# Kernel optimization log

Hardware: AMD Instinct MI355X
Metric: run time of the kernel (lower is better)

## Reference

```python
import jax, jax.numpy as jnp
import numpy as np

B, HW, ENC, DEC, ATTN = 512, 196, 2048, 512, 512

def setup_inputs() -> dict:
    key = jax.random.key(0)
    ks = jax.random.split(key, 8)
    s_enc = 1.0 / np.sqrt(ENC)
    s_dec = 1.0 / np.sqrt(DEC)
    s_v = 1.0 / np.sqrt(ATTN)
    return {
        "enc_out": jax.random.normal(ks[0], (B, HW, ENC), dtype=jnp.float32),
        "dec_h": jax.random.normal(ks[1], (B, DEC), dtype=jnp.float32),
        "W_enc": jax.random.uniform(ks[2], (ENC, ATTN), jnp.float32, -s_enc, s_enc),
        "b_enc": jax.random.uniform(ks[3], (ATTN,), jnp.float32, -s_enc, s_enc),
        "W_dec": jax.random.uniform(ks[4], (DEC, ATTN), jnp.float32, -s_dec, s_dec),
        "b_dec": jax.random.uniform(ks[5], (ATTN,), jnp.float32, -s_dec, s_dec),
        "W_v": jax.random.uniform(ks[6], (ATTN,), jnp.float32, -s_v, s_v),
        "b_v": jax.random.uniform(ks[7], (), jnp.float32, -s_v, s_v),
    }

def reference(enc_out, dec_h, W_enc, b_enc, W_dec, b_dec, W_v, b_v):
    # attn1: [B, HW, ATTN]; attn2: [B, 1, ATTN]
    attn1 = jnp.einsum('bse,ea->bsa', enc_out, W_enc) + b_enc
    attn2 = (dec_h @ W_dec + b_dec)[:, None, :]
    score = jax.nn.relu(attn1 + attn2)
    logits = jnp.einsum('bsa,a->bs', score, W_v) + b_v  # [B, HW]
    alpha = jax.nn.softmax(logits, axis=1)
    context_vec = jnp.einsum('bs,bse->be', alpha, enc_out)
    return (context_vec, alpha)
```

## Files before the change

kernel.cpp:

```cpp
#include <hip/hip_runtime.h>
#include <hip/hip_bf16.h>
#include <cstdint>
#include <cstddef>

#define B_    512
#define HW_   196
#define ENC_  2048
#define DEC_  512
#define ATTN_ 512
#define M_    (B_*HW_)

typedef __attribute__((ext_vector_type(8))) short short8;
typedef __attribute__((ext_vector_type(4))) float f32x4;

__device__ __forceinline__ unsigned short f2bf(float x) {
  __bf16 b = (__bf16)x;
  return __builtin_bit_cast(unsigned short, b);
}
__device__ __forceinline__ unsigned int cvt2(float x, float y) {
  return (unsigned)f2bf(x) | ((unsigned)f2bf(y) << 16);
}

__device__ __forceinline__ void gload_lds16(const void* g, void* l) {
  __builtin_amdgcn_global_load_lds(
      (const __attribute__((address_space(1))) void*)g,
      (__attribute__((address_space(3))) void*)l, 16, 0, 0);
}

__global__ __launch_bounds__(256)
void k_convert(const float* __restrict__ in, unsigned short* __restrict__ out) {
  const size_t total  = (size_t)M_ * ENC_;
  const size_t stride = (size_t)gridDim.x * 256 * 8;
  for (size_t i = ((size_t)blockIdx.x * 256 + threadIdx.x) * 8; i < total; i += stride) {
    const float4 a = *reinterpret_cast<const float4*>(in + i);
    const float4 b = *reinterpret_cast<const float4*>(in + i + 4);
    uint4 o;
    o.x = cvt2(a.x, a.y);  o.y = cvt2(a.z, a.w);
    o.z = cvt2(b.x, b.y);  o.w = cvt2(b.z, b.w);
    *reinterpret_cast<uint4*>(out + i) = o;
  }
}

__global__ __launch_bounds__(256)
void k_attn2(const float* __restrict__ dec_h, const float* __restrict__ Wdec,
             const float* __restrict__ bdec, const float* __restrict__ benc,
             float* __restrict__ attn2p) {
  __shared__ float dh[DEC_];
  const int b = blockIdx.x;
  const int t = threadIdx.x;
  dh[t]       = dec_h[b*DEC_ + t];
  dh[t + 256] = dec_h[b*DEC_ + t + 256];
  __syncthreads();
  #pragma unroll
  for (int rep = 0; rep < 2; ++rep) {
    const int a = t + rep*256;
    float acc = bdec[a] + benc[a];
    #pragma unroll 8
    for (int k = 0; k < DEC_; ++k)
      acc = fmaf(dh[k], Wdec[(size_t)k*ATTN_ + a], acc);
    attn2p[(size_t)b*ATTN_ + a] = acc;
  }
}

__global__ __launch_bounds__(256)
void k_transpose(const float* __restrict__ Wenc, unsigned short* __restrict__ WencT) {
  __shared__ float tile[32][33];
  const int e0 = blockIdx.x * 32;
  const int a0 = blockIdx.y * 32;
  const int t  = threadIdx.x;
  const int li = t >> 5;
  const int lj = t & 31;
  #pragma unroll
  for (int rep = 0; rep < 4; ++rep) {
    const int i = li + rep*8;
    tile[i][lj] = Wenc[(size_t)(e0 + i)*ATTN_ + a0 + lj];
  }
  __syncthreads();
  #pragma unroll
  for (int rep = 0; rep < 4; ++rep) {
    const int ar = li + rep*8;
    WencT[(size_t)(a0 + ar)*ENC_ + e0 + lj] = f2bf(tile[lj][ar]);
  }
}

#define NKS 64

__global__ __launch_bounds__(512, 1)
void k_gemm8(const unsigned short* __restrict__ ench,
             const unsigned short* __restrict__ WencT,
             const float* __restrict__ attn2p,
             const float* __restrict__ Wv,
             float* __restrict__ partials) {
  __shared__ unsigned short A4[4][256*32];
  __shared__ unsigned short B4[4][128*32];

  const int tid = threadIdx.x;
  const int id  = blockIdx.x;
  const int xcd  = id & 7;
  const int rest = id >> 3;
  const int nb   = rest & 3;
  const int mblk = (rest >> 2)*8 + xcd;
  const int r0 = mblk * 256;
  const int n0 = nb * 128;

  const int w  = tid >> 6;
  const int l  = tid & 63;
  const int wm = w >> 1, wn = w & 1;
  const int lrow = l & 15;
  const int kg   = l >> 4;

  const unsigned short* aBase[2];
  #pragma unroll
  for (int i = 0; i < 2; ++i) {
    const int j  = tid + i*512;
    const int rr = j >> 2;
    const int kc = (j & 3) ^ ((rr >> 1) & 3);
    aBase[i] = ench + (size_t)(r0 + rr)*ENC_ + kc*8;
  }
  const unsigned short* bBase;
  {
    const int rr = tid >> 2;
    const int kc = (tid & 3) ^ ((rr >> 1) & 3);
    bBase = WencT + (size_t)(n0 + rr)*ENC_ + kc*8;
  }

  int aOff[4], bOff[4];
  #pragma unroll
  for (int mi = 0; mi < 4; ++mi) {
    const int R  = wm*64 + mi*16 + lrow;
    const int jc = kg ^ ((R >> 1) & 3);
    aOff[mi] = (R*4 + jc) * 8;
  }
  #pragma unroll
  for (int ni = 0; ni < 4; ++ni) {
    const int R  = wn*64 + ni*16 + lrow;
    const int jc = kg ^ ((R >> 1) & 3);
    bOff[ni] = (R*4 + jc) * 8;
  }

  f32x4 acc[4][4];
  #pragma unroll
  for (int mi = 0; mi < 4; ++mi)
    #pragma unroll
    for (int ni = 0; ni < 4; ++ni)
      acc[mi][ni] = (f32x4){0.f, 0.f, 0.f, 0.f};

#define STAGE(KT) do {                                                         \
    const size_t _ko = (size_t)(KT)*32;                                        \
    const int _bw = (KT) & 3;                                                  \
    gload_lds16(aBase[0] + _ko, &A4[_bw][tid*8]);                              \
    gload_lds16(aBase[1] + _ko, &A4[_bw][4096 + tid*8]);                       \
    gload_lds16(bBase    + _ko, &B4[_bw][tid*8]);                              \
  } while (0)

  STAGE(0); STAGE(1); STAGE(2);
  asm volatile("s_waitcnt vmcnt(6)" ::: "memory");
  __builtin_amdgcn_s_barrier();

  for (int kt = 0; kt < NKS; ++kt) {
    const unsigned short* aB = &A4[kt & 3][0];
    const unsigned short* bB = &B4[kt & 3][0];
    short8 aF[4], bF[4];
    #pragma unroll
    for (int mi = 0; mi < 4; ++mi)
      aF[mi] = *reinterpret_cast<const short8*>(&aB[aOff[mi]]);
    #pragma unroll
    for (int ni = 0; ni < 4; ++ni)
      bF[ni] = *reinterpret_cast<const short8*>(&bB[bOff[ni]]);
    if (kt + 3 < NKS) STAGE(kt + 3);
    __builtin_amdgcn_s_barrier();
    __builtin_amdgcn_s_setprio(1);
    #pragma unroll
    for (int mi = 0; mi < 4; ++mi)
      #pragma unroll
      for (int ni = 0; ni < 4; ++ni)
        acc[mi][ni] = __builtin_amdgcn_mfma_f32_16x16x32_bf16(
            aF[mi], bF[ni], acc[mi][ni], 0, 0, 0);
    __builtin_amdgcn_s_setprio(0);
    if (kt < NKS - 3)      { asm volatile("s_waitcnt vmcnt(6)" ::: "memory"); }
    else if (kt == NKS - 3){ asm volatile("s_waitcnt vmcnt(3)" ::: "memory"); }
    else if (kt == NKS - 2){ asm volatile("s_waitcnt vmcnt(0)" ::: "memory"); }
    __builtin_amdgcn_s_barrier();
  }
#undef STAGE

  __syncthreads();
  float* plog = reinterpret_cast<float*>(&A4[0][0]);
  float wvv[4];
  #pragma unroll
  for (int ni = 0; ni < 4; ++ni) wvv[ni] = Wv[n0 + wn*64 + ni*16 + lrow];
  #pragma unroll
  for (int mi = 0; mi < 4; ++mi) {
    #pragma unroll
    for (int j = 0; j < 4; ++j) {
      const int row_local = wm*64 + mi*16 + kg*4 + j;
      const int r  = r0 + row_local;
      const int bb = r / HW_;
      const float* a2 = attn2p + (size_t)bb*ATTN_ + n0 + wn*64;
      float s = 0.f;
      #pragma unroll
      for (int ni = 0; ni < 4; ++ni) {
        float v = acc[mi][ni][j] + a2[ni*16 + lrow];
        v = fmaxf(v, 0.f);
        s = fmaf(v, wvv[ni], s);
      }
      s += __shfl_xor(s, 1);
      s += __shfl_xor(s, 2);
      s += __shfl_xor(s, 4);
      s += __shfl_xor(s, 8);
      if (lrow == 0) plog[row_local*2 + wn] = s;
    }
  }
  __syncthreads();
  if (tid < 256)
    partials[(size_t)(r0 + tid)*4 + nb] = plog[tid*2] + plog[tid*2 + 1];
}

#define BM 128
#define BN 128
#define BK 32
#define LDA 40
#define NT (ENC_/BK)
__device__ __forceinline__ int invswz8(int p) {
  const int b2 = ((p >> 2) ^ (p >> 4)) & 1;
  const int b1 = ((p >> 1) ^ (p >> 3)) & 1;
  const int b0 = (p ^ (p >> 2) ^ (p >> 4)) & 1;
  return (p & ~7) | (b2 << 2) | (b1 << 1) | b0;
}
__global__ __launch_bounds__(256)
void k_gemm_logits_f32(const float* __restrict__ enc,
                       const unsigned short* __restrict__ WencT,
                       const float* __restrict__ attn2p,
                       const float* __restrict__ Wv,
                       float* __restrict__ partials) {
  __shared__ unsigned short As[BM*LDA];
  __shared__ unsigned short Bs[2][BN*BK];
  __shared__ float plog[BM][2];
  const int tid  = threadIdx.x;
  const int id   = blockIdx.x;
  const int xcd  = id & 7;
  const int rest = id >> 3;
  const int nb   = rest & 3;
  const int mblk = (rest >> 2) * 8 + xcd;
  const int r0 = mblk * BM;
  const int n0 = nb * BN;
  const int arow  = tid >> 1;
  const int ahalf = (tid & 1) << 4;
  const float* aptr = enc + (size_t)(r0 + arow)*ENC_ + ahalf;
  const unsigned short* bbase = WencT + (size_t)n0*ENC_;
  const int w  = tid >> 6;
  const int l  = tid & 63;
  const int wm = w >> 1, wn = w & 1;
  const int lrow = l & 15;
  const int kg   = l >> 4;
  const int lk8  = kg << 3;
  const int g4   = kg << 2;
  f32x4 acc[4][4];
  #pragma unroll
  for (int mi = 0; mi < 4; ++mi)
    #pragma unroll
    for (int ni = 0; ni < 4; ++ni)
      acc[mi][ni] = (f32x4){0.f, 0.f, 0.f, 0.f};
  float4 ar[4];
  #pragma unroll
  for (int i = 0; i < 4; ++i) ar[i] = *reinterpret_cast<const float4*>(aptr + i*4);
  #pragma unroll
  for (int r = 0; r < 2; ++r) {
    const int p = r*256 + tid;
    const int c = invswz8(p);
    gload_lds16(bbase + (size_t)(c >> 2)*ENC_ + (c & 3)*8, &Bs[0][p*8]);
  }
  for (int kt = 0; kt < NT; ++kt) {
    {
      unsigned int pk[8];
      #pragma unroll
      for (int i = 0; i < 4; ++i) {
        pk[2*i]   = cvt2(ar[i].x, ar[i].y);
        pk[2*i+1] = cvt2(ar[i].z, ar[i].w);
      }
      uint4* da = reinterpret_cast<uint4*>(&As[arow*LDA + ahalf]);
      da[0] = make_uint4(pk[0], pk[1], pk[2], pk[3]);
      da[1] = make_uint4(pk[4], pk[5], pk[6], pk[7]);
    }
    __syncthreads();
    if (kt + 1 < NT) {
      const float* ap = aptr + (kt + 1)*BK;
      #pragma unroll
      for (int i = 0; i < 4; ++i) ar[i] = *reinterpret_cast<const float4*>(ap + i*4);
      const int k0n = (kt + 1)*BK;
      unsigned short* bdst = Bs[(kt + 1) & 1];
      #pragma unroll
      for (int r = 0; r < 2; ++r) {
        const int p = r*256 + tid;
        const int c = invswz8(p);
        gload_lds16(bbase + (size_t)(c >> 2)*ENC_ + k0n + (c & 3)*8, &bdst[p*8]);
      }
    }
    const unsigned short* bsc = Bs[kt & 1];
    short8 aF[4], bF[4];
    #pragma unroll
    for (int mi = 0; mi < 4; ++mi)
      aF[mi] = *reinterpret_cast<const short8*>(&As[(wm*64 + mi*16 + lrow)*LDA + lk8]);
    #pragma unroll
    for (int ni = 0; ni < 4; ++ni) {
      const int cr = ((wn*64 + ni*16 + lrow) << 2) + kg;
      const int pr = cr ^ ((cr >> 2) & 7);
      bF[ni] = *reinterpret_cast<const short8*>(&bsc[pr << 3]);
    }
    #pragma unroll
    for (int mi = 0; mi < 4; ++mi)
      #pragma unroll
      for (int ni = 0; ni < 4; ++ni)
        acc[mi][ni] = __builtin_amdgcn_mfma_f32_16x16x32_bf16(aF[mi], bF[ni], acc[mi][ni], 0, 0, 0);
    __syncthreads();
  }
  float wvv[4];
  #pragma unroll
  for (int ni = 0; ni < 4; ++ni) wvv[ni] = Wv[n0 + wn*64 + ni*16 + lrow];
  #pragma unroll
  for (int mi = 0; mi < 4; ++mi) {
    #pragma unroll
    for (int j = 0; j < 4; ++j) {
      const int row_local = wm*64 + mi*16 + g4 + j;
      const int r  = r0 + row_local;
      const int bb = r / HW_;
      const float* a2 = attn2p + (size_t)bb*ATTN_ + n0 + wn*64;
      float s = 0.f;
      #pragma unroll
      for (int ni = 0; ni < 4; ++ni) {
        float v = acc[mi][ni][j] + a2[ni*16 + lrow];
        v = fmaxf(v, 0.f);
        s = fmaf(v, wvv[ni], s);
      }
      s += __shfl_xor(s, 1);
      s += __shfl_xor(s, 2);
      s += __shfl_xor(s, 4);
      s += __shfl_xor(s, 8);
      if (lrow == 0) plog[row_local][wn] = s;
    }
  }
  __syncthreads();
  if (tid < BM)
    partials[(size_t)(r0 + tid)*4 + nb] = plog[tid][0] + plog[tid][1];
}

__global__ __launch_bounds__(64)
void k_softmax(const float* __restrict__ partials, const float* __restrict__ bvp,
               float* __restrict__ alpha) {
  const int b = blockIdx.x;
  const int t = threadIdx.x;
  const float bv = bvp[0];
  float lg[4];
  #pragma unroll
  for (int i = 0; i < 4; ++i) {
    const int s = t + i*64;
    if (s < HW_) {
      const float4 p = *reinterpret_cast<const float4*>(&partials[(size_t)(b*HW_ + s)*4]);
      lg[i] = p.x + p.y + p.z + p.w + bv;
    } else lg[i] = -INFINITY;
  }
  float mx = fmaxf(fmaxf(lg[0], lg[1]), fmaxf(lg[2], lg[3]));
  #pragma unroll
  for (int off = 32; off; off >>= 1) mx = fmaxf(mx, __shfl_xor(mx, off));
  float sum = 0.f;
  #pragma unroll
  for (int i = 0; i < 4; ++i) { lg[i] = expf(lg[i] - mx); sum += lg[i]; }
  #pragma unroll
  for (int off = 32; off; off >>= 1) sum += __shfl_xor(sum, off);
  const float inv = 1.0f / sum;
  #pragma unroll
  for (int i = 0; i < 4; ++i) {
    const int s = t + i*64;
    if (s < HW_) alpha[b*HW_ + s] = lg[i] * inv;
  }
}

__global__ __launch_bounds__(256)
void k_context_bf16(const unsigned short* __restrict__ ench,
                    const float* __restrict__ alpha, float* __restrict__ ctx) {
  __shared__ float al[HW_];
  const int b = blockIdx.x;
  const int t = threadIdx.x;
  if (t < HW_) al[t] = alpha[b*HW_ + t];
  __syncthreads();
  const unsigned short* base = ench + (size_t)b*HW_*ENC_ + t*8;
  float acc[8] = {0.f,0.f,0.f,0.f,0.f,0.f,0.f,0.f};
  #pragma unroll 2
  for (int s = 0; s < HW_; ++s) {
    const uint4 v = *reinterpret_cast<const uint4*>(base + (size_t)s*ENC_);
    const float a = al[s];
    const unsigned u[4] = {v.x, v.y, v.z, v.w};
    #pragma unroll
    for (int q = 0; q < 4; ++q) {
      const float lo = __builtin_bit_cast(float, u[q] << 16);
      const float hi = __builtin_bit_cast(float, u[q] & 0xffff0000u);
      acc[2*q]   = fmaf(a, lo, acc[2*q]);
      acc[2*q+1] = fmaf(a, hi, acc[2*q+1]);
    }
  }
  float4* o = reinterpret_cast<float4*>(&ctx[(size_t)b*ENC_ + t*8]);
  o[0] = make_float4(acc[0], acc[1], acc[2], acc[3]);
  o[1] = make_float4(acc[4], acc[5], acc[6], acc[7]);
}

__global__ __launch_bounds__(256)
void k_context_f32(const float* __restrict__ enc, const float* __restrict__ alpha,
                   float* __restrict__ ctx) {
  __shared__ float al[HW_];
  const int bi = blockIdx.x;
  const int b  = bi >> 1;
  const int e0 = (bi & 1) << 10;
  const int t  = threadIdx.x;
  if (t < HW_) al[t] = alpha[b*HW_ + t];
  __syncthreads();
  const float* base = enc + (size_t)b*HW_*ENC_ + e0 + t*4;
  float4 acc = {0.f, 0.f, 0.f, 0.f};
  #pragma unroll 4
  for (int s = 0; s < HW_; ++s) {
    const float a = al[s];
    const float4 v = *reinterpret_cast<const float4*>(base + (size_t)s*ENC_);
    acc.x = fmaf(a, v.x, acc.x);
    acc.y = fmaf(a, v.y, acc.y);
    acc.z = fmaf(a, v.z, acc.z);
    acc.w = fmaf(a, v.w, acc.w);
  }
  *reinterpret_cast<float4*>(&ctx[(size_t)b*ENC_ + e0 + t*4]) = acc;
}

extern "C" void kernel_launch(void* const* d_in, const int* in_sizes, int n_in,
                              void* d_out, int out_size, void* d_ws, size_t ws_size,
                              hipStream_t stream) {
  const float* enc   = (const float*)d_in[0];
  const float* dec_h = (const float*)d_in[1];
  const float* Wenc  = (const float*)d_in[2];
  const float* benc  = (const float*)d_in[3];
  const float* Wdec  = (const float*)d_in[4];
  const float* bdec  = (const float*)d_in[5];
  const float* Wv    = (const float*)d_in[6];
  const float* bv    = (const float*)d_in[7];

  float* ctx   = (float*)d_out;
  float* alpha = (float*)d_out + (size_t)B_*ENC_;

  char* ws = (char*)d_ws;
  float*          attn2p   = (float*)ws;
  unsigned short* WencT    = (unsigned short*)(ws + (1u << 20));
  float*          partials = (float*)(ws + 3u*(1u << 20));
  unsigned short* ench     = (unsigned short*)(ws + 5u*(1u << 20));
  const size_t needed = 5u*(1u << 20) + (size_t)M_*ENC_*sizeof(unsigned short);
  const bool big = (ws_size >= needed);

  hipLaunchKernelGGL(k_attn2,     dim3(B_),                dim3(256), 0, stream,
                     dec_h, Wdec, bdec, benc, attn2p);
  hipLaunchKernelGGL(k_transpose, dim3(ENC_/32, ATTN_/32), dim3(256), 0, stream,
                     Wenc, WencT);
  if (big) {
    hipLaunchKernelGGL(k_convert,   dim3(2048),            dim3(256), 0, stream,
                       enc, ench);
    hipLaunchKernelGGL(k_gemm8,     dim3(1568),            dim3(512), 0, stream,
                       ench, WencT, attn2p, Wv, partials);
    hipLaunchKernelGGL(k_softmax,   dim3(B_),              dim3(64),  0, stream,
                       partials, bv, alpha);
    hipLaunchKernelGGL(k_context_bf16, dim3(B_),           dim3(256), 0, stream,
                       ench, alpha, ctx);
  } else {
    hipLaunchKernelGGL(k_gemm_logits_f32, dim3(3136),      dim3(256), 0, stream,
                       enc, WencT, attn2p, Wv, partials);
    hipLaunchKernelGGL(k_softmax,   dim3(B_),              dim3(64),  0, stream,
                       partials, bv, alpha);
    hipLaunchKernelGGL(k_context_f32, dim3(1024),          dim3(256), 0, stream,
                       enc, alpha, ctx);
  }
}
```

Measured before the change: 743.5 us.

## Enlarge bf16 GEMM tile to 256x256 with double-buffered B fragments

The main bf16 logits GEMM now uses a 256x256 output tile per 512-thread block instead of 256x128, arranged as 2x4 waves of 128x64. This halves the number of blocks and the re-reads of the A (encoder) operand. The K loop is restructured so B fragments for the next step are prefetched into registers while A fragments are loaded one at a time inside the MFMA loop. Each block now holds 8x4 accumulators and uses more LDS, so occupancy drops and register pressure rises. The partial-logit buffer shrinks to two N-chunks per row, and a matching softmax variant is added.

Measured after the change: 741.2 us. No clear change (-0.3%).

```diff
diff --git a/kernel.cpp b/kernel.cpp
--- a/kernel.cpp
+++ b/kernel.cpp
@@ -92,55 +92,49 @@
              const float* __restrict__ Wv,
              float* __restrict__ partials) {
   __shared__ unsigned short A4[4][256*32];
-  __shared__ unsigned short B4[4][128*32];
+  __shared__ unsigned short B4[4][256*32];
 
   const int tid = threadIdx.x;
   const int id  = blockIdx.x;
   const int xcd  = id & 7;
   const int rest = id >> 3;
-  const int nb   = rest & 3;
-  const int mblk = (rest >> 2)*8 + xcd;
+  const int nb   = rest & 1;
+  const int mblk = (rest >> 1)*8 + xcd;
   const int r0 = mblk * 256;
-  const int n0 = nb * 128;
+  const int n0 = nb * 256;
 
   const int w  = tid >> 6;
   const int l  = tid & 63;
-  const int wm = w >> 1, wn = w & 1;
+  const int wm = w >> 2, wn = w & 3;
   const int lrow = l & 15;
   const int kg   = l >> 4;
 
-  const unsigned short* aBase[2];
+  const unsigned short* aSrc[2];
+  const unsigned short* bSrc[2];
   #pragma unroll
   for (int i = 0; i < 2; ++i) {
     const int j  = tid + i*512;
     const int rr = j >> 2;
     const int kc = (j & 3) ^ ((rr >> 1) & 3);
-    aBase[i] = ench + (size_t)(r0 + rr)*ENC_ + kc*8;
-  }
-  const unsigned short* bBase;
-  {
-    const int rr = tid >> 2;
-    const int kc = (tid & 3) ^ ((rr >> 1) & 3);
-    bBase = WencT + (size_t)(n0 + rr)*ENC_ + kc*8;
-  }
-
-  int aOff[4], bOff[4];
-  #pragma unroll
-  for (int mi = 0; mi < 4; ++mi) {
-    const int R  = wm*64 + mi*16 + lrow;
-    const int jc = kg ^ ((R >> 1) & 3);
-    aOff[mi] = (R*4 + jc) * 8;
+    aSrc[i] = ench  + (size_t)(r0 + rr)*ENC_ + kc*8;
+    bSrc[i] = WencT + (size_t)(n0 + rr)*ENC_ + kc*8;
+  }
+
+  int aOff[8], bOff[4];
+  #pragma unroll
+  for (int mi = 0; mi < 8; ++mi) {
+    const int R = wm*128 + mi*16 + lrow;
+    aOff[mi] = (R*4 + (kg ^ ((R >> 1) & 3))) * 8;
   }
   #pragma unroll
   for (int ni = 0; ni < 4; ++ni) {
-    const int R  = wn*64 + ni*16 + lrow;
-    const int jc = kg ^ ((R >> 1) & 3);
-    bOff[ni] = (R*4 + jc) * 8;
-  }
-
-  f32x4 acc[4][4];
-  #pragma unroll
-  for (int mi = 0; mi < 4; ++mi)
+    const int C = wn*64 + ni*16 + lrow;
+    bOff[ni] = (C*4 + (kg ^ ((C >> 1) & 3))) * 8;
+  }
+
+  f32x4 acc[8][4];
+  #pragma unroll
+  for (int mi = 0; mi < 8; ++mi)
     #pragma unroll
     for (int ni = 0; ni < 4; ++ni)
       acc[mi][ni] = (f32x4){0.f, 0.f, 0.f, 0.f};
@@ -148,40 +142,52 @@
 #define STAGE(KT) do {                                                         \
     const size_t _ko = (size_t)(KT)*32;                                        \
     const int _bw = (KT) & 3;                                                  \
-    gload_lds16(aBase[0] + _ko, &A4[_bw][tid*8]);                              \
-    gload_lds16(aBase[1] + _ko, &A4[_bw][4096 + tid*8]);                       \
-    gload_lds16(bBase    + _ko, &B4[_bw][tid*8]);                              \
+    gload_lds16(aSrc[0] + _ko, &A4[_bw][tid*8]);                               \
+    gload_lds16(aSrc[1] + _ko, &A4[_bw][4096 + tid*8]);                        \
+    gload_lds16(bSrc[0] + _ko, &B4[_bw][tid*8]);                               \
+    gload_lds16(bSrc[1] + _ko, &B4[_bw][4096 + tid*8]);                        \
   } while (0)
 
   STAGE(0); STAGE(1); STAGE(2);
-  asm volatile("s_waitcnt vmcnt(6)" ::: "memory");
+  asm volatile("s_waitcnt vmcnt(4)" ::: "memory");
   __builtin_amdgcn_s_barrier();
 
-  for (int kt = 0; kt < NKS; ++kt) {
-    const unsigned short* aB = &A4[kt & 3][0];
-    const unsigned short* bB = &B4[kt & 3][0];
-    short8 aF[4], bF[4];
-    #pragma unroll
-    for (int mi = 0; mi < 4; ++mi)
-      aF[mi] = *reinterpret_cast<const short8*>(&aB[aOff[mi]]);
-    #pragma unroll
-    for (int ni = 0; ni < 4; ++ni)
-      bF[ni] = *reinterpret_cast<const short8*>(&bB[bOff[ni]]);
-    if (kt + 3 < NKS) STAGE(kt + 3);
-    __builtin_amdgcn_s_barrier();
-    __builtin_amdgcn_s_setprio(1);
-    #pragma unroll
-    for (int mi = 0; mi < 4; ++mi)
-      #pragma unroll
-      for (int ni = 0; ni < 4; ++ni)
-        acc[mi][ni] = __builtin_amdgcn_mfma_f32_16x16x32_bf16(
-            aF[mi], bF[ni], acc[mi][ni], 0, 0, 0);
-    __builtin_amdgcn_s_setprio(0);
-    if (kt < NKS - 3)      { asm volatile("s_waitcnt vmcnt(6)" ::: "memory"); }
-    else if (kt == NKS - 3){ asm volatile("s_waitcnt vmcnt(3)" ::: "memory"); }
-    else if (kt == NKS - 2){ asm volatile("s_waitcnt vmcnt(0)" ::: "memory"); }
-    __builtin_amdgcn_s_barrier();
-  }
+  short8 bE[4], bO[4];
+  #pragma unroll
+  for (int ni = 0; ni < 4; ++ni)
+    bE[ni] = *reinterpret_cast<const short8*>(&B4[0][bOff[ni]]);
+
+#define STEP(KT, BC, BN, DOSTAGE, VM) do {                                     \
+    if (DOSTAGE) STAGE((KT) + 3);                                              \
+    if ((KT) + 1 < NKS) {                                                      \
+      _Pragma("unroll")                                                        \
+      for (int ni = 0; ni < 4; ++ni)                                           \
+        BN[ni] = *reinterpret_cast<const short8*>(&B4[((KT)+1) & 3][bOff[ni]]);\
+    }                                                                          \
+    __builtin_amdgcn_s_setprio(1);                                             \
+    _Pragma("unroll")                                                          \
+    for (int mi = 0; mi < 8; ++mi) {                                           \
+      const short8 aC = *reinterpret_cast<const short8*>(&A4[(KT) & 3][aOff[mi]]); \
+      _Pragma("unroll")                                                        \
+      for (int ni = 0; ni < 4; ++ni)                                           \
+        acc[mi][ni] = __builtin_amdgcn_mfma_f32_16x16x32_bf16(                 \
+            aC, BC[ni], acc[mi][ni], 0, 0, 0);                                 \
+    }                                                                          \
+    __builtin_amdgcn_s_setprio(0);                                             \
+    if ((VM) == 4)      { asm volatile("s_waitcnt vmcnt(4)" ::: "memory"); }   \
+    else if ((VM) == 0) { asm volatile("s_waitcnt vmcnt(0)" ::: "memory"); }   \
+    __builtin_amdgcn_s_barrier();                                              \
+  } while (0)
+
+  for (int kt = 0; kt < 60; kt += 2) {
+    STEP(kt,     bE, bO, true, 4);
+    STEP(kt + 1, bO, bE, true, 4);
+  }
+  STEP(60, bE, bO, true,  4);
+  STEP(61, bO, bE, false, 0);
+  STEP(62, bE, bO, false, -1);
+  STEP(63, bO, bE, false, -1);
+#undef STEP
 #undef STAGE
 
   __syncthreads();
@@ -190,10 +196,10 @@
   #pragma unroll
   for (int ni = 0; ni < 4; ++ni) wvv[ni] = Wv[n0 + wn*64 + ni*16 + lrow];
   #pragma unroll
-  for (int mi = 0; mi < 4; ++mi) {
+  for (int mi = 0; mi < 8; ++mi) {
     #pragma unroll
     for (int j = 0; j < 4; ++j) {
-      const int row_local = wm*64 + mi*16 + kg*4 + j;
+      const int row_local = wm*128 + mi*16 + kg*4 + j;
       const int r  = r0 + row_local;
       const int bb = r / HW_;
       const float* a2 = attn2p + (size_t)bb*ATTN_ + n0 + wn*64;
@@ -208,12 +214,14 @@
       s += __shfl_xor(s, 2);
       s += __shfl_xor(s, 4);
       s += __shfl_xor(s, 8);
-      if (lrow == 0) plog[row_local*2 + wn] = s;
+      if (lrow == 0) plog[row_local*4 + wn] = s;
     }
   }
   __syncthreads();
-  if (tid < 256)
-    partials[(size_t)(r0 + tid)*4 + nb] = plog[tid*2] + plog[tid*2 + 1];
+  if (tid < 256) {
+    const float4 p = *reinterpret_cast<const float4*>(&plog[tid*4]);
+    partials[(size_t)(r0 + tid)*2 + nb] = p.x + p.y + p.z + p.w;
+  }
 }
 
 #define BM 128
@@ -345,8 +353,39 @@
 }
 
 __global__ __launch_bounds__(64)
-void k_softmax(const float* __restrict__ partials, const float* __restrict__ bvp,
-               float* __restrict__ alpha) {
+void k_softmax2(const float* __restrict__ partials, const float* __restrict__ bvp,
+                float* __restrict__ alpha) {
+  const int b = blockIdx.x;
+  const int t = threadIdx.x;
+  const float bv = bvp[0];
+  float lg[4];
+  #pragma unroll
+  for (int i = 0; i < 4; ++i) {
+    const int s = t + i*64;
+    if (s < HW_) {
+      const float2 p = *reinterpret_cast<const float2*>(&partials[(size_t)(b*HW_ + s)*2]);
+      lg[i] = p.x + p.y + bv;
+    } else lg[i] = -INFINITY;
+  }
+  float mx = fmaxf(fmaxf(lg[0], lg[1]), fmaxf(lg[2], lg[3]));
+  #pragma unroll
+  for (int off = 32; off; off >>= 1) mx = fmaxf(mx, __shfl_xor(mx, off));
+  float sum = 0.f;
+  #pragma unroll
+  for (int i = 0; i < 4; ++i) { lg[i] = expf(lg[i] - mx); sum += lg[i]; }
+  #pragma unroll
+  for (int off = 32; off; off >>= 1) sum += __shfl_xor(sum, off);
+  const float inv = 1.0f / sum;
+  #pragma unroll
+  for (int i = 0; i < 4; ++i) {
+    const int s = t + i*64;
+    if (s < HW_) alpha[b*HW_ + s] = lg[i] * inv;
+  }
+}
+
+__global__ __launch_bounds__(64)
+void k_softmax4(const float* __restrict__ partials, const float* __restrict__ bvp,
+                float* __restrict__ alpha) {
   const int b = blockIdx.x;
   const int t = threadIdx.x;
   const float bv = bvp[0];
@@ -457,16 +496,16 @@
   if (big) {
     hipLaunchKernelGGL(k_convert,   dim3(2048),            dim3(256), 0, stream,
                        enc, ench);
-    hipLaunchKernelGGL(k_gemm8,     dim3(1568),            dim3(512), 0, stream,
+    hipLaunchKernelGGL(k_gemm8,     dim3(784),             dim3(512), 0, stream,
                        ench, WencT, attn2p, Wv, partials);
-    hipLaunchKernelGGL(k_softmax,   dim3(B_),              dim3(64),  0, stream,
+    hipLaunchKernelGGL(k_softmax2,  dim3(B_),              dim3(64),  0, stream,
                        partials, bv, alpha);
     hipLaunchKernelGGL(k_context_bf16, dim3(B_),           dim3(256), 0, stream,
                        ench, alpha, ctx);
   } else {
     hipLaunchKernelGGL(k_gemm_logits_f32, dim3(3136),      dim3(256), 0, stream,
                        enc, WencT, attn2p, Wv, partials);
-    hipLaunchKernelGGL(k_softmax,   dim3(B_),              dim3(64),  0, stream,
+    hipLaunchKernelGGL(k_softmax4,  dim3(B_),              dim3(64),  0, stream,
                        partials, bv, alpha);
     hipLaunchKernelGGL(k_context_f32, dim3(1024),          dim3(256), 0, stream,
                        enc, alpha, ctx);
```
